# Kernel optimization log

Hardware: AMD Instinct MI355X
Metric: run time of the kernel (lower is better)

The kernel has to match this reference:

```python
import jax, jax.numpy as jnp
import numpy as np

B, N, FEAT, HID, H = 4, 2048, 512, 512, 8
HD = HID // H  # head_dim = 64


def rotate_half(x):
    # pairs along last dim: (x1, x2) -> (-x2, x1), interleaved
    x = x.reshape(*x.shape[:-1], -1, 2)
    x1, x2 = x[..., 0], x[..., 1]
    return jnp.stack((-x2, x1), axis=-1).reshape(*x.shape[:-2], -1)


def apply_rope(freqs, t):
    # freqs: [2, B, 1, N, HD] broadcasting over heads; t: [B, H, N, HD]
    return t * freqs[0] + rotate_half(t) * freqs[1]


def setup_inputs() -> dict:
    key = jax.random.key(0)
    ks = jax.random.split(key, 12)
    s = 0.02
    return {
        "x0": jax.random.normal(ks[0], (B, N, FEAT), jnp.float32),
        "x1": jax.random.normal(ks[1], (B, N, FEAT), jnp.float32),
        "encoding0": jax.random.normal(ks[2], (2, B, 1, N, HD), jnp.float32),
        "encoding1": jax.random.normal(ks[3], (2, B, 1, N, HD), jnp.float32),
        "Wqkv": jax.random.normal(ks[4], (FEAT, 3 * HID), jnp.float32) * s,
        "bqkv": jnp.zeros((3 * HID,), jnp.float32),
        "Wproj": jax.random.normal(ks[5], (HID, HID), jnp.float32) * s,
        "bproj": jnp.zeros((HID,), jnp.float32),
        "W1": jax.random.normal(ks[6], (FEAT + HID, 2 * FEAT), jnp.float32) * s,
        "b1": jnp.zeros((2 * FEAT,), jnp.float32),
        "ln_g": jnp.ones((2 * FEAT,), jnp.float32),
        "ln_b": jnp.zeros((2 * FEAT,), jnp.float32),
        "W2": jax.random.normal(ks[7], (2 * FEAT, FEAT), jnp.float32) * s,
        "b2": jnp.zeros((FEAT,), jnp.float32),
    }


def _block(x, enc, Wqkv, bqkv, Wproj, bproj, W1, b1, ln_g, ln_b, W2, b2):
    b, n, _ = x.shape
    qkv = x @ Wqkv + bqkv                                   # [B,N,3*HID]
    qkv = qkv.reshape(b, n, H, HD, 3).transpose(0, 2, 1, 3, 4)  # [B,H,N,HD,3]
    q, k, v = qkv[..., 0], qkv[..., 1], qkv[..., 2]
    q = apply_rope(enc, q)
    k = apply_rope(enc, k)
    scale = q.shape[-1] ** (-0.5)
    attn = jax.nn.softmax(jnp.einsum('bhid,bhjd->bhij', q, k) * scale, axis=-1)
    o = jnp.einsum('bhij,bhjd->bhid', attn, v)              # [B,H,N,HD]
    message = o.transpose(0, 2, 1, 3).reshape(b, n, HID) @ Wproj + bproj
    h = jnp.concatenate([x, message], axis=-1) @ W1 + b1    # [B,N,2*FEAT]
    mu = h.mean(-1, keepdims=True)
    var = ((h - mu) ** 2).mean(-1, keepdims=True)
    h = (h - mu) * jax.lax.rsqrt(var + 1e-5) * ln_g + ln_b
    return x + jax.nn.gelu(h, approximate=False) @ W2 + b2


def reference(x0, x1, encoding0, encoding1, Wqkv, bqkv, Wproj, bproj, W1, b1, ln_g, ln_b, W2, b2):
    p = (Wqkv, bqkv, Wproj, bproj, W1, b1, ln_g, ln_b, W2, b2)
    return (_block(x0, encoding0, *p), _block(x1, encoding1, *p))
```

## Files before the change

### kernel.cpp

```cpp
#include <hip/hip_runtime.h>
#include <hip/hip_bf16.h>

typedef __attribute__((ext_vector_type(8))) short   short8v;
typedef __attribute__((ext_vector_type(4))) short   short4v;
typedef __attribute__((ext_vector_type(8))) __bf16  bf16x8;
typedef __attribute__((ext_vector_type(4))) __bf16  bf16x4;
typedef __attribute__((ext_vector_type(4))) float   f32x4;

constexpr int Nn = 2048;

#define GLOAD_LDS(src, dst) \
  __builtin_amdgcn_global_load_lds((__attribute__((address_space(1))) unsigned int*)(src), \
                                   (__attribute__((address_space(3))) unsigned int*)(dst), 16, 0, 0)

#if __has_builtin(__builtin_amdgcn_exp2f)
#define EXP2F(x) __builtin_amdgcn_exp2f(x)
#else
#define EXP2F(x) exp2f(x)
#endif

#if __has_builtin(__builtin_amdgcn_mfma_f32_16x16x16bf16_1k)
#define HAVE_MFMA16 1
#define MFMA16(a, b, c) __builtin_amdgcn_mfma_f32_16x16x16bf16_1k(a, b, c, 0, 0, 0)
#else
#define HAVE_MFMA16 0
#endif

__device__ __forceinline__ unsigned pack_bf16(float lo, float hi) {
  union { __bf16 h[2]; unsigned u; } t;
  t.h[0] = (__bf16)lo; t.h[1] = (__bf16)hi;
  return t.u;
}

template<int AMODE, int BMODE, int EPI>
__global__ __launch_bounds__(256)
void gemm_mfma(const __bf16* __restrict__ A, const __bf16* __restrict__ A2,
               const __bf16* __restrict__ BT, const __bf16* __restrict__ BT2,
               const float* __restrict__ bias,
               const float* __restrict__ resid0, const float* __restrict__ resid1,
               float* __restrict__ Cf, __bf16* __restrict__ Cb, __bf16* __restrict__ Vt,
               int lda, int ldb, int ldb2, int ldc, int K1, int K)
{
  __shared__ __align__(16) __bf16 As[2][4096];
  __shared__ __align__(16) __bf16 Bs[2][4096];
  const int tid = threadIdx.x;
  const int w = tid >> 6, l = tid & 63;
  const int wr = w >> 1, wc = w & 1;
  const int lr = l & 15, lg = l >> 4;
  const int row0 = blockIdx.x * 128, col0 = blockIdx.y * 128;

  f32x4 acc[4][4];
#pragma unroll
  for (int i = 0; i < 4; ++i)
#pragma unroll
    for (int j = 0; j < 4; ++j) acc[i][j] = (f32x4){0.f, 0.f, 0.f, 0.f};

  const int srow = l >> 2;
  const int skk  = (((l & 3) ^ ((l >> 3) & 3))) * 8;

  auto stage = [&](int k0, int b) {
#pragma unroll
    for (int s = w; s < 8; s += 4) {
      const int m = s * 16 + srow;
      const __bf16* src;
      if constexpr (AMODE == 0) {
        src = A + (size_t)(row0 + m) * lda + k0 + skk;
      } else {
        const int gk = k0 + skk;
        src = (gk < K1) ? A  + (size_t)(row0 + m) * lda + gk
                        : A2 + (size_t)(row0 + m) * lda + (gk - K1);
      }
      GLOAD_LDS(src, &As[b][s * 512]);
    }
#pragma unroll
    for (int s = w; s < 8; s += 4) {
      const int n = s * 16 + srow;
      const __bf16* src;
      if constexpr (BMODE == 0) {
        src = BT + (size_t)(col0 + n) * ldb + k0 + skk;
      } else {
        const int gk = k0 + skk;
        src = (gk < K1) ? BT  + (size_t)(col0 + n) * ldb + gk
                        : BT2 + (size_t)(col0 + n) * ldb2 + (gk - K1);
      }
      GLOAD_LDS(src, &Bs[b][s * 512]);
    }
  };

  const int nt = K >> 5;
  stage(0, 0);

  const int rsl = (lr >> 1) & 3;

  for (int t = 0; t < nt; ++t) {
    const int p = t & 1;
    if (t + 1 < nt) {
      stage((t + 1) * 32, 1 - p);
      asm volatile("s_waitcnt vmcnt(4)" ::: "memory");
    } else {
      asm volatile("s_waitcnt vmcnt(0)" ::: "memory");
    }
    __builtin_amdgcn_sched_barrier(0);
    __builtin_amdgcn_s_barrier();
    __builtin_amdgcn_sched_barrier(0);
    bf16x8 af[4], bfv[4];
#pragma unroll
    for (int mi = 0; mi < 4; ++mi)
      af[mi] = *(const bf16x8*)&As[p][(wr * 64 + mi * 16 + lr) * 32 + (lg ^ rsl) * 8];
#pragma unroll
    for (int ni = 0; ni < 4; ++ni)
      bfv[ni] = *(const bf16x8*)&Bs[p][(wc * 64 + ni * 16 + lr) * 32 + (lg ^ rsl) * 8];
    __builtin_amdgcn_s_setprio(1);
#pragma unroll
    for (int mi = 0; mi < 4; ++mi)
#pragma unroll
      for (int ni = 0; ni < 4; ++ni)
        acc[mi][ni] = __builtin_amdgcn_mfma_f32_16x16x32_bf16(af[mi], bfv[ni], acc[mi][ni], 0, 0, 0);
    __builtin_amdgcn_s_setprio(0);
    __builtin_amdgcn_s_barrier();
  }

  if constexpr (EPI == 4) {
    if (col0 >= 1024) {
      const int b2 = row0 >> 11;
#pragma unroll
      for (int mi = 0; mi < 4; ++mi)
#pragma unroll
        for (int ni = 0; ni < 4; ++ni) {
          const int col = col0 + wc * 64 + ni * 16 + lr;
          const int sec = col - 1024, h = sec >> 6, d = sec & 63;
          const int n0 = (row0 + wr * 64 + mi * 16 + lg * 4) & 2047;
          union { __bf16 h4[4]; short4 s4; } u;
#pragma unroll
          for (int r = 0; r < 4; ++r) u.h4[r] = (__bf16)(acc[mi][ni][r] + bias[col]);
          *(short4*)&Vt[(size_t)(b2 * 8 + h) * 131072 + (size_t)d * 2048 + n0] = u.s4;
        }
    } else {
      constexpr float SCQ = 0.125f * 1.44269504089f;
      const float* e = (row0 < 8192) ? resid0 : resid1;
#pragma unroll
      for (int mi = 0; mi < 4; ++mi)
#pragma unroll
        for (int ni = 0; ni < 4; ++ni) {
          const int col = col0 + wc * 64 + ni * 16 + lr;
          const int d = col & 63;
          const float sgn = (col & 1) ? 1.f : -1.f;
          const float scq = (col < 512) ? SCQ : 1.f;
#pragma unroll
          for (int r = 0; r < 4; ++r) {
            const int row = row0 + wr * 64 + mi * 16 + lg * 4 + r;
            const long bn = row & 8191;
            const float f0 = e[bn * 64 + d];
            const float f1 = e[524288 + bn * 64 + d];
            const float vb = acc[mi][ni][r] + bias[col];
            const float pb = __shfl_xor(vb, 1, 64);
            Cb[(size_t)row * 1024 + col] = (__bf16)((vb * f0 + sgn * pb * f1) * scq);
          }
        }
    }
    return;
  }

#pragma unroll
  for (int mi = 0; mi < 4; ++mi)
#pragma unroll
    for (int ni = 0; ni < 4; ++ni) {
      const int col = col0 + wc * 64 + ni * 16 + lr;
#pragma unroll
      for (int r = 0; r < 4; ++r) {
        const int row = row0 + wr * 64 + mi * 16 + lg * 4 + r;
        const float v = acc[mi][ni][r];
        if constexpr (EPI == 1) {
          Cb[(size_t)row * ldc + col] = (__bf16)(v + bias[col]);
        } else if constexpr (EPI == 3) {
          Cb[(size_t)row * ldc + col] = (__bf16)v;
        } else {
          const float rv = (float)Vt[(size_t)row * ldc + col];
          Cf[(size_t)row * ldc + col] = v + bias[col] + rv;
        }
      }
    }
}

__global__ __launch_bounds__(256, 2)
void fa_k(const __bf16* __restrict__ QK, const __bf16* __restrict__ Vg,
          __bf16* __restrict__ Ob)
{
  constexpr float FIXM = 8.f;
  __shared__ __align__(16) __bf16 Ks[3][4096];
  __shared__ __align__(16) __bf16 Vs[3][4096];
  const int tid = threadIdx.x;
  const int w = tid >> 6, l = tid & 63;
  const int lr = l & 15, lg = l >> 4;
  const int bid = blockIdx.x;
  const int qi = (bid >> 3) & 7;
  const int bh = (bid & 7) * 8 + (bid >> 6);
  const int b2 = bh >> 3, h = bh & 7;
  const __bf16* Qp = QK + (size_t)b2 * 2048 * 1024 + h * 64;
  const __bf16* Kp = Qp + 512;
  const __bf16* Vp = Vg + (size_t)bh * 131072;
  const int q0 = qi * 256 + w * 64;

  bf16x8 qf[4][2];
#pragma unroll
  for (int nf = 0; nf < 4; ++nf)
#pragma unroll
    for (int kk = 0; kk < 2; ++kk)
      qf[nf][kk] = *(const bf16x8*)&Qp[(size_t)(q0 + nf * 16 + lr) * 1024 + kk * 32 + lg * 8];

  f32x4 oacc[4][4];
#pragma unroll
  for (int i = 0; i < 4; ++i)
#pragma unroll
    for (int j = 0; j < 4; ++j) oacc[i][j] = (f32x4){0.f, 0.f, 0.f, 0.f};
  float rs[4] = {0.f, 0.f, 0.f, 0.f};

#if !HAVE_MFMA16
  const int Sa = (lg & 1) * 32 + lr, Sb2x = Sa + 16;
  const bool hi = (lg >> 1) & 1;
#endif

  auto stage = [&](int kv0, int b) {
#pragma unroll
    for (int i = 0; i < 2; ++i) {
      const int s = w + 4 * i;
      const int g = s * 64 + l, r = g >> 3, c = g & 7;
      GLOAD_LDS(Kp + (size_t)(kv0 + r) * 1024 + ((c ^ (r & 7)) * 8), &Ks[b][s * 512]);
      GLOAD_LDS(Vp + (size_t)r * 2048 + kv0 + ((c ^ (r & 7)) * 8), &Vs[b][s * 512]);
    }
  };

  stage(0, 0);
  stage(64, 1);
  asm volatile("s_waitcnt vmcnt(4)" ::: "memory");
  __builtin_amdgcn_sched_barrier(0);

  for (int t = 0; t < 32; ++t) {
    const int p = t % 3;
    __builtin_amdgcn_s_barrier();
    __builtin_amdgcn_sched_barrier(0);
    if (t + 2 < 32) stage((t + 2) * 64, (t + 2) % 3);

    f32x4 sacc[4][4];
#pragma unroll
    for (int i = 0; i < 4; ++i)
#pragma unroll
      for (int j = 0; j < 4; ++j) sacc[i][j] = (f32x4){0.f, 0.f, 0.f, 0.f};
#pragma unroll
    for (int kk = 0; kk < 2; ++kk) {
      bf16x8 ka[4];
#pragma unroll
      for (int mf = 0; mf < 4; ++mf)
        ka[mf] = *(const bf16x8*)&Ks[p][(mf * 16 + lr) * 64 + (((kk * 4 + lg) ^ (lr & 7)) * 8)];
      __builtin_amdgcn_s_setprio(1);
#pragma unroll
      for (int mf = 0; mf < 4; ++mf)
#pragma unroll
        for (int nf = 0; nf < 4; ++nf)
          sacc[mf][nf] = __builtin_amdgcn_mfma_f32_16x16x32_bf16(ka[mf], qf[nf][kk], sacc[mf][nf], 0, 0, 0);
      __builtin_amdgcn_s_setprio(0);
    }

    unsigned pkk[4][4][2];
#pragma unroll
    for (int nf = 0; nf < 4; ++nf) {
#pragma unroll
      for (int mf = 0; mf < 4; ++mf) {
        const float p0 = EXP2F(sacc[mf][nf][0] - FIXM);
        const float p1 = EXP2F(sacc[mf][nf][1] - FIXM);
        const float p2 = EXP2F(sacc[mf][nf][2] - FIXM);
        const float p3 = EXP2F(sacc[mf][nf][3] - FIXM);
        rs[nf] += (p0 + p1) + (p2 + p3);
        pkk[mf][nf][0] = pack_bf16(p0, p1);
        pkk[mf][nf][1] = pack_bf16(p2, p3);
      }
    }

#if HAVE_MFMA16
#pragma unroll
    for (int ks = 0; ks < 4; ++ks) {
      bf16x4 va[4];
#pragma unroll
      for (int mo = 0; mo < 4; ++mo) {
        const int g = (ks * 2 + (lg >> 1)) ^ (lr & 7);
        va[mo] = *(const bf16x4*)&Vs[p][(mo * 16 + lr) * 64 + g * 8 + (lg & 1) * 4];
      }
      __builtin_amdgcn_s_setprio(1);
#pragma unroll
      for (int mo = 0; mo < 4; ++mo)
#pragma unroll
        for (int nf = 0; nf < 4; ++nf)
          oacc[mo][nf] = MFMA16(__builtin_bit_cast(short4v, va[mo]),
                                __builtin_bit_cast(short4v, pkk[ks][nf]),
                                oacc[mo][nf]);
      __builtin_amdgcn_s_setprio(0);
    }
#else
#pragma unroll
    for (int kf = 0; kf < 2; ++kf) {
      bf16x8 va[4];
#pragma unroll
      for (int mo = 0; mo < 4; ++mo) {
        const int g = ((kf * 4 + lg) ^ (lr & 7));
        va[mo] = *(const bf16x8*)&Vs[p][(mo * 16 + lr) * 64 + g * 8];
      }
      bf16x8 bfr[4];
#pragma unroll
      for (int nf = 0; nf < 4; ++nf) {
        const unsigned s0 = hi ? pkk[kf * 2 + 1][nf][0] : pkk[kf * 2][nf][0];
        const unsigned s1 = hi ? pkk[kf * 2 + 1][nf][1] : pkk[kf * 2][nf][1];
        union { unsigned u[4]; bf16x8 v; } ub;
        ub.u[0] = (unsigned)__shfl((int)s0, Sa, 64);
        ub.u[1] = (unsigned)__shfl((int)s1, Sa, 64);
        ub.u[2] = (unsigned)__shfl((int)s0, Sb2x, 64);
        ub.u[3] = (unsigned)__shfl((int)s1, Sb2x, 64);
        bfr[nf] = ub.v;
      }
      __builtin_amdgcn_s_setprio(1);
#pragma unroll
      for (int mo = 0; mo < 4; ++mo)
#pragma unroll
        for (int nf = 0; nf < 4; ++nf)
          oacc[mo][nf] = __builtin_amdgcn_mfma_f32_16x16x32_bf16(va[mo], bfr[nf], oacc[mo][nf], 0, 0, 0);
      __builtin_amdgcn_s_setprio(0);
    }
#endif
    if (t < 31) {
      if (t + 2 < 32) asm volatile("s_waitcnt vmcnt(4)" ::: "memory");
      else            asm volatile("s_waitcnt vmcnt(0)" ::: "memory");
    }
    __builtin_amdgcn_sched_barrier(0);
  }

#pragma unroll
  for (int nf = 0; nf < 4; ++nf) {
    float ls = rs[nf];
    ls += __shfl_xor(ls, 16, 64);
    ls += __shfl_xor(ls, 32, 64);
    const float inv = 1.f / ls;
    const long row = (long)b2 * 2048 + q0 + nf * 16 + lr;
#pragma unroll
    for (int mo = 0; mo < 4; ++mo) {
      union { __bf16 h4[4]; short4 s4; } u;
#pragma unroll
      for (int r = 0; r < 4; ++r) u.h4[r] = (__bf16)(oacc[mo][nf][r] * inv);
      *(short4*)&Ob[row * 512 + h * 64 + mo * 16 + lg * 4] = u.s4;
    }
  }
}

__global__ __launch_bounds__(256)
void conv_f32_bf16_k(const float* __restrict__ s, __bf16* __restrict__ d)
{
  const long i = ((long)blockIdx.x * 256 + threadIdx.x) * 4;
  const float4 v = *(const float4*)&s[i];
  union { __bf16 h[4]; short4 sv; } u;
  u.h[0] = (__bf16)v.x; u.h[1] = (__bf16)v.y; u.h[2] = (__bf16)v.z; u.h[3] = (__bf16)v.w;
  *(short4*)&d[i] = u.sv;
}

__global__ __launch_bounds__(256)
void conv2_k(const float* __restrict__ x0, const float* __restrict__ x1,
             __bf16* __restrict__ d)
{
  const int bid = blockIdx.x;
  const float* s = (bid < 4096) ? x0 : x1;
  __bf16* dd = d + ((bid < 4096) ? 0 : 4194304);
  const long i = ((long)(bid & 4095) * 256 + threadIdx.x) * 4;
  const float4 v = *(const float4*)&s[i];
  union { __bf16 h[4]; short4 sv; } u;
  u.h[0] = (__bf16)v.x; u.h[1] = (__bf16)v.y; u.h[2] = (__bf16)v.z; u.h[3] = (__bf16)v.w;
  *(short4*)&dd[i] = u.sv;
}

__global__ __launch_bounds__(256)
void prep_wt_k(const float* __restrict__ Wqkv, const float* __restrict__ W1,
               const float* __restrict__ W2,
               __bf16* __restrict__ WqkvT, __bf16* __restrict__ W1T,
               __bf16* __restrict__ W2T)
{
  const int bid = blockIdx.x;
  const float* W; __bf16* WT; int K, N, bx, by; bool perm = false;
  if (bid < 768)       { W = Wqkv; WT = WqkvT; K = 512;  N = 1536; bx = bid % 48;          by = bid / 48;          perm = true; }
  else if (bid < 1792) { W = W1;   WT = W1T;   K = 1024; N = 1024; bx = (bid - 768) % 32;  by = (bid - 768) / 32; }
  else                 { W = W2;   WT = W2T;   K = 1024; N = 512;  bx = (bid - 1792) % 16; by = (bid - 1792) / 16; }
  __shared__ float t[32][33];
  const int n0 = bx * 32, k0 = by * 32;
  const int tx = threadIdx.x & 31, ty = threadIdx.x >> 5;
  for (int i = ty; i < 32; i += 8)
    t[i][tx] = W[(size_t)(k0 + i) * N + n0 + tx];
  __syncthreads();
  for (int i = ty; i < 32; i += 8) {
    int drow = n0 + i;
    if (perm) {
      const int h = drow / 192, rem = drow % 192;
      drow = (rem % 3) * 512 + h * 64 + rem / 3;
    }
    WT[(size_t)drow * K + k0 + tx] = (__bf16)t[tx][i];
  }
}

__global__ void bperm_k(const float* __restrict__ b, float* __restrict__ bp)
{
  const int i = blockIdx.x * 256 + threadIdx.x;
  if (i < 1536) {
    const int h = i / 192, rem = i % 192;
    bp[(rem % 3) * 512 + h * 64 + rem / 3] = b[i];
  }
}

__global__ __launch_bounds__(256)
void bfuse_k(const float* __restrict__ b1, const float* __restrict__ bproj,
             const float* __restrict__ W1, float* __restrict__ b1f)
{
  const int n = blockIdx.x * 256 + threadIdx.x;
  float s = b1[n];
  for (int m = 0; m < 512; ++m)
    s += bproj[m] * W1[(size_t)(512 + m) * 1024 + n];
  b1f[n] = s;
}

__global__ __launch_bounds__(256)
void ln_gelu_k(__bf16* __restrict__ Hb, const float* __restrict__ g,
               const float* __restrict__ be)
{
  __bf16* row = Hb + (size_t)blockIdx.x * 1024;
  const int tid = threadIdx.x, w = tid >> 6, l = tid & 63;
  __shared__ float ps[4][2];
  union { __bf16 h[4]; short4 sv; } u;
  u.sv = *(const short4*)&row[tid * 4];
  float v[4];
  float s = 0.f, sq = 0.f;
#pragma unroll
  for (int i = 0; i < 4; ++i) {
    v[i] = (float)u.h[i];
    s += v[i]; sq += v[i] * v[i];
  }
#pragma unroll
  for (int d = 32; d > 0; d >>= 1) {
    s  += __shfl_xor(s, d, 64);
    sq += __shfl_xor(sq, d, 64);
  }
  if (l == 0) { ps[w][0] = s; ps[w][1] = sq; }
  __syncthreads();
  s  = ps[0][0] + ps[1][0] + ps[2][0] + ps[3][0];
  sq = ps[0][1] + ps[1][1] + ps[2][1] + ps[3][1];
  const float mu = s * (1.f / 1024.f);
  const float var = sq * (1.f / 1024.f) - mu * mu;
  const float rstd = rsqrtf(var + 1e-5f);
#pragma unroll
  for (int i = 0; i < 4; ++i) {
    const int c = tid * 4 + i;
    const float y = (v[i] - mu) * rstd * g[c] + be[c];
    u.h[i] = (__bf16)(0.5f * y * (1.f + erff(y * 0.70710678118f)));
  }
  *(short4*)&row[tid * 4] = u.sv;
}

extern "C" void kernel_launch(void* const* d_in, const int* in_sizes, int n_in,
                              void* d_out, int out_size, void* d_ws, size_t ws_size,
                              hipStream_t stream)
{
  const float* x0   = (const float*)d_in[0];
  const float* x1   = (const float*)d_in[1];
  const float* enc0 = (const float*)d_in[2];
  const float* enc1 = (const float*)d_in[3];
  const float* Wqkv  = (const float*)d_in[4];
  const float* bqkv  = (const float*)d_in[5];
  const float* Wproj = (const float*)d_in[6];
  const float* bproj = (const float*)d_in[7];
  const float* W1    = (const float*)d_in[8];
  const float* b1    = (const float*)d_in[9];
  const float* ln_g  = (const float*)d_in[10];
  const float* ln_b  = (const float*)d_in[11];
  const float* W2    = (const float*)d_in[12];
  const float* b2    = (const float*)d_in[13];

  __bf16* wsb = (__bf16*)d_ws;
  __bf16* xb      = wsb;
  __bf16* WqkvT   = wsb + 8388608;
  __bf16* Wproj_b = wsb + 9175040;
  __bf16* W1T     = wsb + 9437184;
  __bf16* W2T     = wsb + 10485760;
  float*  bqkvp   = (float*)(wsb + 11010048);
  __bf16* qkvb    = wsb + 11013120;
  __bf16* Vt      = wsb + 27790336;
  __bf16* Ob      = wsb + 36178944;
  __bf16* WfT     = wsb + 44567552;
  float*  b1f     = (float*)(wsb + 45091840);
  __bf16* hb      = qkvb;

  prep_wt_k<<<2304, 256, 0, stream>>>(Wqkv, W1, W2, WqkvT, W1T, W2T);
  bperm_k<<<6, 256, 0, stream>>>(bqkv, bqkvp);
  conv_f32_bf16_k<<<256, 256, 0, stream>>>(Wproj, Wproj_b);
  gemm_mfma<0, 0, 3><<<dim3(8, 4), 256, 0, stream>>>(
      W1T + 512, nullptr, Wproj_b, nullptr, nullptr, nullptr, nullptr,
      nullptr, WfT, nullptr, 1024, 512, 0, 512, 0, 512);
  bfuse_k<<<4, 256, 0, stream>>>(b1, bproj, W1, b1f);

  conv2_k<<<8192, 256, 0, stream>>>(x0, x1, xb);

  gemm_mfma<0, 0, 4><<<dim3(128, 12), 256, 0, stream>>>(
      xb, nullptr, WqkvT, nullptr, bqkvp, enc0, enc1, nullptr, qkvb, Vt,
      512, 512, 0, 1024, 0, 512);
  fa_k<<<512, 256, 0, stream>>>(qkvb, Vt, Ob);
  gemm_mfma<1, 1, 1><<<dim3(128, 8), 256, 0, stream>>>(
      xb, Ob, W1T, WfT, b1f, nullptr, nullptr, nullptr, hb, nullptr,
      512, 1024, 512, 1024, 512, 1024);
  ln_gelu_k<<<16384, 256, 0, stream>>>(hb, ln_g, ln_b);
  gemm_mfma<0, 0, 2><<<dim3(128, 4), 256, 0, stream>>>(
      hb, nullptr, W2T, nullptr, b2, nullptr, nullptr, (float*)d_out, nullptr, xb,
      1024, 1024, 0, 512, 0, 1024);
}
```

Before: 309.6 us.

## Interleave softmax exp with PV MFMAs and merge small prep kernels

In the flash-attention loop, the exp/pack of P is now computed per k-slice, directly before the MFMAs that consume it, instead of for all slices up front. This lowers live registers and lets the scheduler overlap transcendental work with matrix ops. Separately, three tiny setup kernels (Wproj conversion, bias permute, fused bias) are merged into one launch to cut launch overhead.

```diff
diff --git a/kernel.cpp b/kernel.cpp
--- a/kernel.cpp
+++ b/kernel.cpp
@@ -261,7 +261,38 @@
       __builtin_amdgcn_s_setprio(0);
     }
 
-    unsigned pkk[4][4][2];
+#if HAVE_MFMA16
+#pragma unroll
+    for (int ks = 0; ks < 4; ++ks) {
+      unsigned pkk[4][2];
+#pragma unroll
+      for (int nf = 0; nf < 4; ++nf) {
+        const float p0 = EXP2F(sacc[ks][nf][0] - FIXM);
+        const float p1 = EXP2F(sacc[ks][nf][1] - FIXM);
+        const float p2 = EXP2F(sacc[ks][nf][2] - FIXM);
+        const float p3 = EXP2F(sacc[ks][nf][3] - FIXM);
+        rs[nf] += (p0 + p1) + (p2 + p3);
+        pkk[nf][0] = pack_bf16(p0, p1);
+        pkk[nf][1] = pack_bf16(p2, p3);
+      }
+      bf16x4 va[4];
+#pragma unroll
+      for (int mo = 0; mo < 4; ++mo) {
+        const int g = (ks * 2 + (lg >> 1)) ^ (lr & 7);
+        va[mo] = *(const bf16x4*)&Vs[p][(mo * 16 + lr) * 64 + g * 8 + (lg & 1) * 4];
+      }
+      __builtin_amdgcn_s_setprio(1);
+#pragma unroll
+      for (int mo = 0; mo < 4; ++mo)
+#pragma unroll
+        for (int nf = 0; nf < 4; ++nf)
+          oacc[mo][nf] = MFMA16(__builtin_bit_cast(short4v, va[mo]),
+                                __builtin_bit_cast(short4v, pkk[nf]),
+                                oacc[mo][nf]);
+      __builtin_amdgcn_s_setprio(0);
+    }
+#else
+    unsigned pkkf[4][4][2];
 #pragma unroll
     for (int nf = 0; nf < 4; ++nf) {
 #pragma unroll
@@ -271,31 +302,10 @@
         const float p2 = EXP2F(sacc[mf][nf][2] - FIXM);
         const float p3 = EXP2F(sacc[mf][nf][3] - FIXM);
         rs[nf] += (p0 + p1) + (p2 + p3);
-        pkk[mf][nf][0] = pack_bf16(p0, p1);
-        pkk[mf][nf][1] = pack_bf16(p2, p3);
-      }
-    }
-
-#if HAVE_MFMA16
-#pragma unroll
-    for (int ks = 0; ks < 4; ++ks) {
-      bf16x4 va[4];
-#pragma unroll
-      for (int mo = 0; mo < 4; ++mo) {
-        const int g = (ks * 2 + (lg >> 1)) ^ (lr & 7);
-        va[mo] = *(const bf16x4*)&Vs[p][(mo * 16 + lr) * 64 + g * 8 + (lg & 1) * 4];
-      }
-      __builtin_amdgcn_s_setprio(1);
-#pragma unroll
-      for (int mo = 0; mo < 4; ++mo)
-#pragma unroll
-        for (int nf = 0; nf < 4; ++nf)
-          oacc[mo][nf] = MFMA16(__builtin_bit_cast(short4v, va[mo]),
-                                __builtin_bit_cast(short4v, pkk[ks][nf]),
-                                oacc[mo][nf]);
-      __builtin_amdgcn_s_setprio(0);
-    }
-#else
+        pkkf[mf][nf][0] = pack_bf16(p0, p1);
+        pkkf[mf][nf][1] = pack_bf16(p2, p3);
+      }
+    }
 #pragma unroll
     for (int kf = 0; kf < 2; ++kf) {
       bf16x8 va[4];
@@ -307,8 +317,8 @@
       bf16x8 bfr[4];
 #pragma unroll
       for (int nf = 0; nf < 4; ++nf) {
-        const unsigned s0 = hi ? pkk[kf * 2 + 1][nf][0] : pkk[kf * 2][nf][0];
-        const unsigned s1 = hi ? pkk[kf * 2 + 1][nf][1] : pkk[kf * 2][nf][1];
+        const unsigned s0 = hi ? pkkf[kf * 2 + 1][nf][0] : pkkf[kf * 2][nf][0];
+        const unsigned s1 = hi ? pkkf[kf * 2 + 1][nf][1] : pkkf[kf * 2][nf][1];
         union { unsigned u[4]; bf16x8 v; } ub;
         ub.u[0] = (unsigned)__shfl((int)s0, Sa, 64);
         ub.u[1] = (unsigned)__shfl((int)s1, Sa, 64);
@@ -347,16 +357,6 @@
       *(short4*)&Ob[row * 512 + h * 64 + mo * 16 + lg * 4] = u.s4;
     }
   }
-}
-
-__global__ __launch_bounds__(256)
-void conv_f32_bf16_k(const float* __restrict__ s, __bf16* __restrict__ d)
-{
-  const long i = ((long)blockIdx.x * 256 + threadIdx.x) * 4;
-  const float4 v = *(const float4*)&s[i];
-  union { __bf16 h[4]; short4 sv; } u;
-  u.h[0] = (__bf16)v.x; u.h[1] = (__bf16)v.y; u.h[2] = (__bf16)v.z; u.h[3] = (__bf16)v.w;
-  *(short4*)&d[i] = u.sv;
 }
 
 __global__ __launch_bounds__(256)
@@ -400,24 +400,33 @@
   }
 }
 
-__global__ void bperm_k(const float* __restrict__ b, float* __restrict__ bp)
-{
-  const int i = blockIdx.x * 256 + threadIdx.x;
-  if (i < 1536) {
-    const int h = i / 192, rem = i % 192;
-    bp[(rem % 3) * 512 + h * 64 + rem / 3] = b[i];
-  }
-}
-
 __global__ __launch_bounds__(256)
-void bfuse_k(const float* __restrict__ b1, const float* __restrict__ bproj,
-             const float* __restrict__ W1, float* __restrict__ b1f)
-{
-  const int n = blockIdx.x * 256 + threadIdx.x;
-  float s = b1[n];
-  for (int m = 0; m < 512; ++m)
-    s += bproj[m] * W1[(size_t)(512 + m) * 1024 + n];
-  b1f[n] = s;
+void prep_small_k(const float* __restrict__ Wproj, const float* __restrict__ bqkv,
+                  const float* __restrict__ b1, const float* __restrict__ bproj,
+                  const float* __restrict__ W1,
+                  __bf16* __restrict__ Wproj_b, float* __restrict__ bqkvp,
+                  float* __restrict__ b1f)
+{
+  const int bid = blockIdx.x, tid = threadIdx.x;
+  if (bid < 256) {
+    const long i = ((long)bid * 256 + tid) * 4;
+    const float4 v = *(const float4*)&Wproj[i];
+    union { __bf16 h[4]; short4 sv; } u;
+    u.h[0] = (__bf16)v.x; u.h[1] = (__bf16)v.y; u.h[2] = (__bf16)v.z; u.h[3] = (__bf16)v.w;
+    *(short4*)&Wproj_b[i] = u.sv;
+  } else if (bid < 262) {
+    const int i = (bid - 256) * 256 + tid;
+    if (i < 1536) {
+      const int h = i / 192, rem = i % 192;
+      bqkvp[(rem % 3) * 512 + h * 64 + rem / 3] = bqkv[i];
+    }
+  } else {
+    const int n = (bid - 262) * 256 + tid;
+    float s = b1[n];
+    for (int m = 0; m < 512; ++m)
+      s += bproj[m] * W1[(size_t)(512 + m) * 1024 + n];
+    b1f[n] = s;
+  }
 }
 
 __global__ __launch_bounds__(256)
@@ -491,12 +500,11 @@
   __bf16* hb      = qkvb;
 
   prep_wt_k<<<2304, 256, 0, stream>>>(Wqkv, W1, W2, WqkvT, W1T, W2T);
-  bperm_k<<<6, 256, 0, stream>>>(bqkv, bqkvp);
-  conv_f32_bf16_k<<<256, 256, 0, stream>>>(Wproj, Wproj_b);
+  prep_small_k<<<266, 256, 0, stream>>>(Wproj, bqkv, b1, bproj, W1,
+                                        Wproj_b, bqkvp, b1f);
   gemm_mfma<0, 0, 3><<<dim3(8, 4), 256, 0, stream>>>(
       W1T + 512, nullptr, Wproj_b, nullptr, nullptr, nullptr, nullptr,
       nullptr, WfT, nullptr, 1024, 512, 0, 512, 0, 512);
-  bfuse_k<<<4, 256, 0, stream>>>(b1, bproj, W1, b1f);
 
   conv2_k<<<8192, 256, 0, stream>>>(x0, x1, xb);
 
```

After: 293.6 us. 5.2% less time.
